# Performance work log

Measured on AMD Instinct MI355X. Metric: run time of the kernel, lower is better.

## Reference

```python
import jax, jax.numpy as jnp
import numpy as np

GROUPS = 32
EPS = 1e-5   # nn.GroupNorm default


def group_norm(x, gamma, beta):
    # x: [B, C, H, W]
    b, c, h, w = x.shape
    xg = x.reshape(b, GROUPS, c // GROUPS, h, w)
    mu = jnp.mean(xg, axis=(2, 3, 4), keepdims=True)
    var = jnp.var(xg, axis=(2, 3, 4), keepdims=True)
    xn = ((xg - mu) * jax.lax.rsqrt(var + EPS)).reshape(b, c, h, w)
    return xn * gamma[None, :, None, None] + beta[None, :, None, None]


def conv1x1(x, w, b):
    # x: [B, C, H, W], w: [O, C], b: [O]
    return jnp.einsum('bchw,oc->bohw', x, w) + b[None, :, None, None]


def setup_inputs() -> dict:
    key = jax.random.key(0)
    ks = jax.random.split(key, 10)
    B, C, H, W = 8, 512, 64, 64
    std = 1.0 / np.sqrt(C)
    inp = {
        'x': jax.random.normal(ks[0], (B, C, H, W), dtype=jnp.float32),
        'gn_gamma': jnp.ones((C,), dtype=jnp.float32),
        'gn_beta': jnp.zeros((C,), dtype=jnp.float32),
        'wq': jax.random.normal(ks[1], (C, C), dtype=jnp.float32) * std,
        'bq': jnp.zeros((C,), dtype=jnp.float32),
        'wk': jax.random.normal(ks[2], (C, C), dtype=jnp.float32) * std,
        'bk': jnp.zeros((C,), dtype=jnp.float32),
        'wv': jax.random.normal(ks[3], (C, C), dtype=jnp.float32) * std,
        'bv': jnp.zeros((C,), dtype=jnp.float32),
        'wp': jax.random.normal(ks[4], (C, C), dtype=jnp.float32) * std,
        'bp': jnp.zeros((C,), dtype=jnp.float32),
    }
    return inp


def reference(x, gn_gamma, gn_beta, wq, bq, wk, bk, wv, bv, wp, bp):
    b, c, hh, ww = x.shape
    n = hh * ww
    h = group_norm(x, gn_gamma, gn_beta)
    q = conv1x1(h, wq, bq).reshape(b, c, n).transpose(0, 2, 1)  # [B, N, C]
    k = conv1x1(h, wk, bk).reshape(b, c, n)                     # [B, C, N]
    v = conv1x1(h, wv, bv).reshape(b, c, n).transpose(0, 2, 1)  # [B, N, C]
    scale = 1.0 / jnp.sqrt(jnp.asarray(c, dtype=x.dtype))
    attn = jax.nn.softmax(jnp.einsum('bnc,bcm->bnm', q, k) * scale, axis=-1)
    out = jnp.einsum('bnm,bmc->bnc', attn, v)                   # [B, N, C]
    out = out.transpose(0, 2, 1).reshape(b, c, hh, ww)
    return x + conv1x1(out, wp, bp)
```

## Files before the change

### kernel.cpp

```cpp
#include <hip/hip_runtime.h>


typedef __attribute__((ext_vector_type(8))) __bf16 bf16x8;
typedef __attribute__((ext_vector_type(4))) float f32x4;
typedef unsigned int u32;

#define DEVICE __device__ __forceinline__

DEVICE void async_copy16(const void* g, void* l) {
  __builtin_amdgcn_global_load_lds(
      (__attribute__((address_space(1))) u32*)(g),
      (__attribute__((address_space(3))) u32*)(l),
      16, 0, 0);
}

__global__ __launch_bounds__(256) void cvt_w(
    const float* __restrict__ w0, const float* __restrict__ w1,
    const float* __restrict__ w2, const float* __restrict__ w3,
    __bf16* __restrict__ o0, __bf16* __restrict__ o1,
    __bf16* __restrict__ o2, __bf16* __restrict__ o3) {
  int idx = blockIdx.x * 256 + threadIdx.x;
  int off = idx * 8;
  int m = off >> 18;
  int r = off & 262143;
  const float* src = m == 0 ? w0 : m == 1 ? w1 : m == 2 ? w2 : w3;
  __bf16* dst = m == 0 ? o0 : m == 1 ? o1 : m == 2 ? o2 : o3;
  float4 a = *(const float4*)(src + r);
  float4 b = *(const float4*)(src + r + 4);
  bf16x8 v = {(__bf16)a.x, (__bf16)a.y, (__bf16)a.z, (__bf16)a.w,
              (__bf16)b.x, (__bf16)b.y, (__bf16)b.z, (__bf16)b.w};
  *(bf16x8*)(dst + r) = v;
}

__global__ __launch_bounds__(256) void gn_stats(const float* __restrict__ x,
                                                float* __restrict__ stats) {
  int bg = blockIdx.x;
  const float* p = x + (size_t)bg * 65536;
  int t = threadIdx.x, lane = t & 63, w = t >> 6;
  float s = 0.f, ss = 0.f;
  for (int i = t; i < 16384; i += 256) {
    float4 v = *(const float4*)(p + i * 4);
    s += v.x + v.y + v.z + v.w;
    ss += v.x * v.x + v.y * v.y + v.z * v.z + v.w * v.w;
  }
#pragma unroll
  for (int off = 32; off; off >>= 1) {
    s += __shfl_xor(s, off);
    ss += __shfl_xor(ss, off);
  }
  __shared__ float rs_[4], rss_[4];
  if (lane == 0) { rs_[w] = s; rss_[w] = ss; }
  __syncthreads();
  if (t == 0) {
    float S = rs_[0] + rs_[1] + rs_[2] + rs_[3];
    float SS = rss_[0] + rss_[1] + rss_[2] + rss_[3];
    float mean = S * (1.0f / 65536.0f);
    float var = SS * (1.0f / 65536.0f) - mean * mean;
    stats[bg * 2] = mean;
    stats[bg * 2 + 1] = rsqrtf(var + 1e-5f);
  }
}

__global__ __launch_bounds__(256) void gn_apply(
    const float* __restrict__ x, const float* __restrict__ gamma,
    const float* __restrict__ beta, const float* __restrict__ stats,
    __bf16* __restrict__ h) {
  int b = blockIdx.z, g = blockIdx.y;
  int n = blockIdx.x * 256 + threadIdx.x;
  const float* px = x + ((size_t)b * 512 + g * 16) * 4096 + n;
  float mean = stats[(b * 32 + g) * 2];
  float rstd = stats[(b * 32 + g) * 2 + 1];
  bf16x8 lo, hi;
#pragma unroll
  for (int c = 0; c < 8; ++c) {
    float v = px[(size_t)c * 4096];
    lo[c] = (__bf16)((v - mean) * rstd * gamma[g * 16 + c] + beta[g * 16 + c]);
  }
#pragma unroll
  for (int c = 0; c < 8; ++c) {
    float v = px[(size_t)(c + 8) * 4096];
    hi[c] = (__bf16)((v - mean) * rstd * gamma[g * 16 + c + 8] + beta[g * 16 + c + 8]);
  }
  __bf16* dst = h + ((size_t)b * 4096 + n) * 512 + g * 16;
  *(bf16x8*)dst = lo;
  *(bf16x8*)(dst + 8) = hi;
}


#define G256_PHASE(BUF, QR, QC, RDA, RDB, STAGE_STMT, TAIL_STMT)               \
  do {                                                                         \
    if (RDA) {                                                                 \
      _Pragma("unroll") for (int fr = 0; fr < 4; ++fr) {                       \
        a[fr][0] = ldA(BUF, (QR)*4 + fr, 0);                                   \
        a[fr][1] = ldA(BUF, (QR)*4 + fr, 1);                                   \
      }                                                                        \
    }                                                                          \
    if (RDB) {                                                                 \
      _Pragma("unroll") for (int fc = 0; fc < 2; ++fc) {                       \
        b[(QC)*2 + fc][0] = ldB(BUF, (QC)*2 + fc, 0);                          \
        b[(QC)*2 + fc][1] = ldB(BUF, (QC)*2 + fc, 1);                          \
      }                                                                        \
    }                                                                          \
    STAGE_STMT;                                                                \
    __builtin_amdgcn_s_barrier();                                              \
    asm volatile("s_waitcnt lgkmcnt(0)" ::: "memory");                         \
    __builtin_amdgcn_sched_barrier(0);                                         \
    __builtin_amdgcn_s_setprio(1);                                             \
    _Pragma("unroll") for (int fr = 0; fr < 4; ++fr)                           \
      _Pragma("unroll") for (int fc = 0; fc < 2; ++fc) {                       \
        acc[(QR)*4 + fr][(QC)*2 + fc] =                                        \
            __builtin_amdgcn_mfma_f32_16x16x32_bf16(                           \
                a[fr][0], b[(QC)*2 + fc][0], acc[(QR)*4 + fr][(QC)*2 + fc],    \
                0, 0, 0);                                                      \
        acc[(QR)*4 + fr][(QC)*2 + fc] =                                        \
            __builtin_amdgcn_mfma_f32_16x16x32_bf16(                           \
                a[fr][1], b[(QC)*2 + fc][1], acc[(QR)*4 + fr][(QC)*2 + fc],    \
                0, 0, 0);                                                      \
      }                                                                        \
    __builtin_amdgcn_s_setprio(0);                                             \
    TAIL_STMT;                                                                 \
    __builtin_amdgcn_sched_barrier(0);                                         \
    __builtin_amdgcn_s_barrier();                                              \
  } while (0)

#define G256_ITER(T0, T1, LAST)                                                \
  G256_PHASE(0, 0, 0, 1, 1, stage(1, 0, 0, (T1)), ((void)0));                  \
  G256_PHASE(0, 0, 1, 0, 1, stage(1, 0, 1, (T1)), ((void)0));                  \
  G256_PHASE(0, 1, 0, 1, 0,                                                    \
             if (!(LAST)) stage(0, 1, 0, (T0) + 2), ((void)0));                \
  G256_PHASE(0, 1, 1, 0, 0,                                                    \
             if (!(LAST)) stage(0, 1, 1, (T0) + 2),                            \
             if (LAST) {                                                       \
               asm volatile("s_waitcnt vmcnt(0)" ::: "memory");                \
             } else {                                                          \
               asm volatile("s_waitcnt vmcnt(4)" ::: "memory");                \
             });                                                               \
  G256_PHASE(1, 0, 0, 1, 1,                                                    \
             if (!(LAST)) stage(0, 0, 0, (T0) + 2), ((void)0));                \
  G256_PHASE(1, 0, 1, 0, 1,                                                    \
             if (!(LAST)) stage(0, 0, 1, (T0) + 2), ((void)0));                \
  G256_PHASE(1, 1, 0, 1, 0,                                                    \
             if (!(LAST)) stage(1, 1, 0, (T1) + 2), ((void)0));                \
  G256_PHASE(1, 1, 1, 0, 0,                                                    \
             if (!(LAST)) stage(1, 1, 1, (T1) + 2),                            \
             if (!(LAST)) {                                                    \
               asm volatile("s_waitcnt vmcnt(4)" ::: "memory");                \
             })

template <int EPI>
__global__ __launch_bounds__(512, 2) void gemm256(
    const __bf16* __restrict__ A, const __bf16* __restrict__ B,
    void* __restrict__ CoutV, int lda, int ldb, int ldc, int nIter, int nTM,
    int nTN, int KS, long sA, long sKA, long sB, long sKB, long sC,
    const float* __restrict__ bias0, const float* __restrict__ bias1,
    const float* __restrict__ resid) {
  __shared__ __bf16 lds_raw[2][2][2][128][64];

  int nwg = gridDim.x, bid = blockIdx.x;
  int qq = nwg >> 3, rr = nwg & 7;
  int xcd = bid & 7, ii = bid >> 3;
  int swz = (xcd < rr ? xcd * (qq + 1) : rr * (qq + 1) + (xcd - rr) * qq) + ii;
  int tn = swz % nTN;
  int tm = (swz / nTN) % nTM;
  int zz = swz / (nTN * nTM);
  int z = zz / KS, ks = zz % KS;
  A += (size_t)z * sA + (size_t)ks * sKA;
  B += (size_t)z * sB + (size_t)ks * sKB;
  __bf16* Cout = (__bf16*)CoutV + (size_t)zz * sC;
  int row0 = tm * 256, col0 = tn * 256;

  int tid = threadIdx.x;
  int wid = tid >> 6, lane = tid & 63;
  int wr = wid >> 2, wc = wid & 3;
  int l15 = lane & 15, l4 = lane >> 4;

  auto stage = [&](int buf, int mat, int half, int kt) {
    const __bf16* src = mat ? B : A;
    int ld = mat ? ldb : lda;
    int rbase = (mat ? col0 : row0) + half * 128;
    char* ldsbase = (char*)lds_raw + (((buf * 2 + mat) * 2 + half) * 16384);
#pragma unroll
    for (int L = 0; L < 2; ++L) {
      int ci = L * 512 + tid;
      int r = ci >> 3, cslot = ci & 7;
      int csrc = cslot ^ (r & 7);
      async_copy16(src + (size_t)(rbase + r) * ld + kt * 64 + csrc * 8,
                   ldsbase + (L * 512 + wid * 64) * 16);
    }
  };
  auto ldA = [&](int buf, int fr, int kh) -> bf16x8 {
    int row = fr * 16 + l15;
    int g = kh * 4 + l4;
    char* base = (char*)lds_raw + (((buf * 2 + 0) * 2 + wr) * 16384);
    return *(const bf16x8*)(base + row * 128 + ((g ^ (row & 7)) * 16));
  };
  auto ldB = [&](int buf, int fc, int kh) -> bf16x8 {
    int row = (wc & 1) * 64 + fc * 16 + l15;
    int g = kh * 4 + l4;
    char* base = (char*)lds_raw + (((buf * 2 + 1) * 2 + (wc >> 1)) * 16384);
    return *(const bf16x8*)(base + row * 128 + ((g ^ (row & 7)) * 16));
  };

  f32x4 acc[8][4] = {};
  bf16x8 a[4][2], b[4][2];

  stage(0, 1, 0, 0);
  stage(0, 1, 1, 0);
  stage(0, 0, 0, 0);
  stage(0, 0, 1, 0);
  stage(1, 1, 0, 1);
  stage(1, 1, 1, 1);
  asm volatile("s_waitcnt vmcnt(4)" ::: "memory");
  __builtin_amdgcn_sched_barrier(0);
  __builtin_amdgcn_s_barrier();

  int it = 0;
  for (; it < nIter - 1; ++it) {
    G256_ITER(2 * it, 2 * it + 1, 0);
  }
  G256_ITER(2 * it, 2 * it + 1, 1);

  int rb = row0 + wr * 128, cb = col0 + wc * 64;
#pragma unroll
  for (int fr = 0; fr < 8; ++fr) {
#pragma unroll
    for (int fc = 0; fc < 4; ++fc) {
      int col = cb + fc * 16 + l15;
      if constexpr (EPI == 3) {
        int r0 = rb + fr * 16 + l4 * 4;
        size_t idx = ((size_t)(r0 >> 12) * 512 + col) * 4096 + (r0 & 4095);
        float4 rv = *(const float4*)(resid + idx);
        float bb = bias0[col];
        float4 ov = {acc[fr][fc][0] + bb + rv.x, acc[fr][fc][1] + bb + rv.y,
                     acc[fr][fc][2] + bb + rv.z, acc[fr][fc][3] + bb + rv.w};
        *(float4*)((float*)CoutV + idx) = ov;
      } else {
        float cbias = 0.f;
        if constexpr (EPI == 1)
          cbias = col < 512 ? bias0[col] : bias1[col - 512];
#pragma unroll
        for (int rg = 0; rg < 4; ++rg) {
          int row = rb + fr * 16 + l4 * 4 + rg;
          float v = acc[fr][fc][rg];
          if constexpr (EPI == 1) v += cbias;
          if constexpr (EPI == 2) v += bias0[row];
          Cout[(size_t)row * ldc + col] = (__bf16)v;
        }
      }
    }
  }
}

__global__ __launch_bounds__(256) void softmax_rows_bf16(__bf16* __restrict__ S) {
  int row = blockIdx.x;
  __bf16* p = S + (size_t)row * 4096;
  int t = threadIdx.x, lane = t & 63, w = t >> 6;
  const float c1 = 0.04419417382415922f * 1.4426950408889634f;
  bf16x8 v0 = *(const bf16x8*)(p + t * 16);
  bf16x8 v1 = *(const bf16x8*)(p + t * 16 + 8);
  float f[16];
  float mx = -3.4e38f;
#pragma unroll
  for (int i = 0; i < 8; ++i) { f[i] = (float)v0[i]; mx = fmaxf(mx, f[i]); }
#pragma unroll
  for (int i = 0; i < 8; ++i) { f[8 + i] = (float)v1[i]; mx = fmaxf(mx, f[8 + i]); }
#pragma unroll
  for (int off = 32; off; off >>= 1) mx = fmaxf(mx, __shfl_xor(mx, off));
  __shared__ float rm[4], rsum[4];
  if (lane == 0) rm[w] = mx;
  __syncthreads();
  float m = fmaxf(fmaxf(rm[0], rm[1]), fmaxf(rm[2], rm[3]));
  float s = 0.f;
#pragma unroll
  for (int i = 0; i < 16; ++i) {
    f[i] = exp2f((f[i] - m) * c1);
    s += f[i];
  }
#pragma unroll
  for (int off = 32; off; off >>= 1) s += __shfl_xor(s, off);
  if (lane == 0) rsum[w] = s;
  __syncthreads();
  float inv = 1.0f / (rsum[0] + rsum[1] + rsum[2] + rsum[3]);
  bf16x8 o0, o1;
#pragma unroll
  for (int i = 0; i < 8; ++i) o0[i] = (__bf16)(f[i] * inv);
#pragma unroll
  for (int i = 0; i < 8; ++i) o1[i] = (__bf16)(f[8 + i] * inv);
  *(bf16x8*)(p + t * 16) = o0;
  *(bf16x8*)(p + t * 16 + 8) = o1;
}

__global__ __launch_bounds__(256) void reduce4(const __bf16* __restrict__ part,
                                               __bf16* __restrict__ out) {
  int z = blockIdx.y;
  size_t e = ((size_t)blockIdx.x * 256 + threadIdx.x) * 8;
  const __bf16* p = part + (size_t)z * 4 * 2097152 + e;
  bf16x8 v0 = *(const bf16x8*)(p);
  bf16x8 v1 = *(const bf16x8*)(p + 2097152);
  bf16x8 v2 = *(const bf16x8*)(p + 2 * 2097152);
  bf16x8 v3 = *(const bf16x8*)(p + 3 * 2097152);
  bf16x8 o;
#pragma unroll
  for (int j = 0; j < 8; ++j)
    o[j] = (__bf16)((float)v0[j] + (float)v1[j] + (float)v2[j] + (float)v3[j]);
  *(bf16x8*)(out + (size_t)z * 2097152 + e) = o;
}

extern "C" void kernel_launch(void* const* d_in, const int* in_sizes, int n_in,
                              void* d_out, int out_size, void* d_ws, size_t ws_size,
                              hipStream_t stream) {
  const float* x = (const float*)d_in[0];
  const float* gamma = (const float*)d_in[1];
  const float* beta = (const float*)d_in[2];
  const float* wq = (const float*)d_in[3];
  const float* bq = (const float*)d_in[4];
  const float* wk = (const float*)d_in[5];
  const float* bk = (const float*)d_in[6];
  const float* wv = (const float*)d_in[7];
  const float* bv = (const float*)d_in[8];
  const float* wp = (const float*)d_in[9];
  const float* bp = (const float*)d_in[10];

  char* p = (char*)d_ws;
  auto alloc = [&](size_t bytes) {
    char* r = p;
    p += (bytes + 255) & ~(size_t)255;
    return r;
  };
  float* stats = (float*)alloc(256 * 2 * 4);
  __bf16* wqkb = (__bf16*)alloc((size_t)1024 * 512 * 2);
  __bf16* wvb = (__bf16*)alloc(512 * 512 * 2);
  __bf16* wpb = (__bf16*)alloc(512 * 512 * 2);
  __bf16* ho = (__bf16*)alloc((size_t)8 * 4096 * 512 * 2);
  __bf16* qk = (__bf16*)alloc((size_t)8 * 4096 * 1024 * 2);
  __bf16* vt = (__bf16*)alloc((size_t)8 * 512 * 4096 * 2);

  const size_t SB = (size_t)4096 * 4096 * 2;
  const size_t PB = (size_t)4 * 4096 * 512 * 2;
  size_t used = (size_t)(p - (char*)d_ws);
  size_t freeb = (ws_size > used) ? ws_size - used : 0;
  int nb = (int)(freeb / (SB + PB));
  if (nb > 8) nb = 8;
  if (nb < 1) nb = 1;
  __bf16* s = (__bf16*)alloc(SB * nb);
  __bf16* pvp = (__bf16*)alloc(PB * nb);

  cvt_w<<<512, 256, 0, stream>>>(wq, wk, wv, wp, wqkb, wqkb + 262144, wvb, wpb);
  gn_stats<<<256, 256, 0, stream>>>(x, stats);
  gn_apply<<<dim3(16, 32, 8), 256, 0, stream>>>(x, gamma, beta, stats, ho);

  gemm256<1><<<dim3(512), 512, 0, stream>>>(
      ho, wqkb, qk, 512, 512, 1024, 4, 128, 4, 1, 0, 0, 0, 0, 0, bq, bk, nullptr);
  gemm256<2><<<dim3(256), 512, 0, stream>>>(
      wvb, ho, vt, 512, 512, 4096, 4, 2, 16, 1, 0, 0, 2097152, 0, 2097152,
      bv, nullptr, nullptr);

  __bf16* o = ho;
  for (int b0 = 0; b0 < 8; b0 += nb) {
    int zb = (8 - b0 < nb) ? (8 - b0) : nb;
    gemm256<0><<<dim3(zb * 256), 512, 0, stream>>>(
        qk + (size_t)b0 * 4194304, qk + (size_t)b0 * 4194304 + 512, s, 1024,
        1024, 4096, 4, 16, 16, 1, 4194304, 0, 4194304, 0, 16777216,
        nullptr, nullptr, nullptr);
    softmax_rows_bf16<<<zb * 4096, 256, 0, stream>>>(s);
    gemm256<0><<<dim3(zb * 128), 512, 0, stream>>>(
        s, vt + (size_t)b0 * 2097152, pvp, 4096, 4096, 512, 8, 16, 2, 4,
        16777216, 1024, 2097152, 1024, 2097152, nullptr, nullptr, nullptr);
    reduce4<<<dim3(1024, zb), 256, 0, stream>>>(pvp, o + (size_t)b0 * 2097152);
  }
  gemm256<3><<<dim3(256), 512, 0, stream>>>(
      o, wpb, d_out, 512, 512, 0, 4, 128, 2, 1, 0, 0, 0, 0, 0, bp, nullptr, x);
}
```

Measured before the change: 609.7 us.

## Split GEMM tile across sixteen waves with 64x64 per-wave subtiles

The 256x256-tile GEMM kernel now launches 1024 threads (16 waves in a 4x4 grid) instead of 512. Each wave computes a 64x64 output subtile instead of 128x64, and each thread issues one async global-to-LDS copy per stage instead of two. The vmcnt waits are lowered to match, and the launch bounds become (1024, 4). The aim is more waves to hide latency and fewer accumulator registers per wave. In exchange, each wave reuses its LDS fragments less, so there are more LDS reads per MFMA, and the strict launch-bounds hint may squeeze registers enough to cause spills.

Measured after the change: 914.8 us. 1.5x slower.

```diff
diff --git a/kernel.cpp b/kernel.cpp
--- a/kernel.cpp
+++ b/kernel.cpp
@@ -90,15 +90,15 @@
 #define G256_PHASE(BUF, QR, QC, RDA, RDB, STAGE_STMT, TAIL_STMT)               \
   do {                                                                         \
     if (RDA) {                                                                 \
-      _Pragma("unroll") for (int fr = 0; fr < 4; ++fr) {                       \
-        a[fr][0] = ldA(BUF, (QR)*4 + fr, 0);                                   \
-        a[fr][1] = ldA(BUF, (QR)*4 + fr, 1);                                   \
+      _Pragma("unroll") for (int fp = 0; fp < 2; ++fp) {                       \
+        a[fp][0] = ldA(BUF, (QR)*2 + fp, 0);                                   \
+        a[fp][1] = ldA(BUF, (QR)*2 + fp, 1);                                   \
       }                                                                        \
     }                                                                          \
     if (RDB) {                                                                 \
-      _Pragma("unroll") for (int fc = 0; fc < 2; ++fc) {                       \
-        b[(QC)*2 + fc][0] = ldB(BUF, (QC)*2 + fc, 0);                          \
-        b[(QC)*2 + fc][1] = ldB(BUF, (QC)*2 + fc, 1);                          \
+      _Pragma("unroll") for (int fp = 0; fp < 2; ++fp) {                       \
+        b[(QC)*2 + fp][0] = ldB(BUF, (QC)*2 + fp, 0);                          \
+        b[(QC)*2 + fp][1] = ldB(BUF, (QC)*2 + fp, 1);                          \
       }                                                                        \
     }                                                                          \
     STAGE_STMT;                                                                \
@@ -106,15 +106,15 @@
     asm volatile("s_waitcnt lgkmcnt(0)" ::: "memory");                         \
     __builtin_amdgcn_sched_barrier(0);                                         \
     __builtin_amdgcn_s_setprio(1);                                             \
-    _Pragma("unroll") for (int fr = 0; fr < 4; ++fr)                           \
-      _Pragma("unroll") for (int fc = 0; fc < 2; ++fc) {                       \
-        acc[(QR)*4 + fr][(QC)*2 + fc] =                                        \
+    _Pragma("unroll") for (int fp = 0; fp < 2; ++fp)                           \
+      _Pragma("unroll") for (int fq = 0; fq < 2; ++fq) {                       \
+        acc[(QR)*2 + fp][(QC)*2 + fq] =                                        \
             __builtin_amdgcn_mfma_f32_16x16x32_bf16(                           \
-                a[fr][0], b[(QC)*2 + fc][0], acc[(QR)*4 + fr][(QC)*2 + fc],    \
+                a[fp][0], b[(QC)*2 + fq][0], acc[(QR)*2 + fp][(QC)*2 + fq],    \
                 0, 0, 0);                                                      \
-        acc[(QR)*4 + fr][(QC)*2 + fc] =                                        \
+        acc[(QR)*2 + fp][(QC)*2 + fq] =                                        \
             __builtin_amdgcn_mfma_f32_16x16x32_bf16(                           \
-                a[fr][1], b[(QC)*2 + fc][1], acc[(QR)*4 + fr][(QC)*2 + fc],    \
+                a[fp][1], b[(QC)*2 + fq][1], acc[(QR)*2 + fp][(QC)*2 + fq],    \
                 0, 0, 0);                                                      \
       }                                                                        \
     __builtin_amdgcn_s_setprio(0);                                             \
@@ -133,7 +133,7 @@
              if (LAST) {                                                       \
                asm volatile("s_waitcnt vmcnt(0)" ::: "memory");                \
              } else {                                                          \
-               asm volatile("s_waitcnt vmcnt(4)" ::: "memory");                \
+               asm volatile("s_waitcnt vmcnt(2)" ::: "memory");                \
              });                                                               \
   G256_PHASE(1, 0, 0, 1, 1,                                                    \
              if (!(LAST)) stage(0, 0, 0, (T0) + 2), ((void)0));                \
@@ -144,11 +144,11 @@
   G256_PHASE(1, 1, 1, 0, 0,                                                    \
              if (!(LAST)) stage(1, 1, 1, (T1) + 2),                            \
              if (!(LAST)) {                                                    \
-               asm volatile("s_waitcnt vmcnt(4)" ::: "memory");                \
+               asm volatile("s_waitcnt vmcnt(2)" ::: "memory");                \
              })
 
 template <int EPI>
-__global__ __launch_bounds__(512, 2) void gemm256(
+__global__ __launch_bounds__(1024, 4) void gemm256(
     const __bf16* __restrict__ A, const __bf16* __restrict__ B,
     void* __restrict__ CoutV, int lda, int ldb, int ldc, int nIter, int nTM,
     int nTN, int KS, long sA, long sKA, long sB, long sKB, long sC,
@@ -179,19 +179,15 @@
     int ld = mat ? ldb : lda;
     int rbase = (mat ? col0 : row0) + half * 128;
     char* ldsbase = (char*)lds_raw + (((buf * 2 + mat) * 2 + half) * 16384);
-#pragma unroll
-    for (int L = 0; L < 2; ++L) {
-      int ci = L * 512 + tid;
-      int r = ci >> 3, cslot = ci & 7;
-      int csrc = cslot ^ (r & 7);
-      async_copy16(src + (size_t)(rbase + r) * ld + kt * 64 + csrc * 8,
-                   ldsbase + (L * 512 + wid * 64) * 16);
-    }
+    int r = tid >> 3, cslot = tid & 7;
+    int csrc = cslot ^ (r & 7);
+    async_copy16(src + (size_t)(rbase + r) * ld + kt * 64 + csrc * 8,
+                 ldsbase + tid * 16);
   };
   auto ldA = [&](int buf, int fr, int kh) -> bf16x8 {
-    int row = fr * 16 + l15;
+    int row = (wr & 1) * 64 + fr * 16 + l15;
     int g = kh * 4 + l4;
-    char* base = (char*)lds_raw + (((buf * 2 + 0) * 2 + wr) * 16384);
+    char* base = (char*)lds_raw + (((buf * 2 + 0) * 2 + (wr >> 1)) * 16384);
     return *(const bf16x8*)(base + row * 128 + ((g ^ (row & 7)) * 16));
   };
   auto ldB = [&](int buf, int fc, int kh) -> bf16x8 {
@@ -201,8 +197,8 @@
     return *(const bf16x8*)(base + row * 128 + ((g ^ (row & 7)) * 16));
   };
 
-  f32x4 acc[8][4] = {};
-  bf16x8 a[4][2], b[4][2];
+  f32x4 acc[4][4] = {};
+  bf16x8 a[2][2], b[4][2];
 
   stage(0, 1, 0, 0);
   stage(0, 1, 1, 0);
@@ -210,7 +206,7 @@
   stage(0, 0, 1, 0);
   stage(1, 1, 0, 1);
   stage(1, 1, 1, 1);
-  asm volatile("s_waitcnt vmcnt(4)" ::: "memory");
+  asm volatile("s_waitcnt vmcnt(2)" ::: "memory");
   __builtin_amdgcn_sched_barrier(0);
   __builtin_amdgcn_s_barrier();
 
@@ -220,9 +216,9 @@
   }
   G256_ITER(2 * it, 2 * it + 1, 1);
 
-  int rb = row0 + wr * 128, cb = col0 + wc * 64;
-#pragma unroll
-  for (int fr = 0; fr < 8; ++fr) {
+  int rb = row0 + wr * 64, cb = col0 + wc * 64;
+#pragma unroll
+  for (int fr = 0; fr < 4; ++fr) {
 #pragma unroll
     for (int fc = 0; fc < 4; ++fc) {
       int col = cb + fc * 16 + l15;
@@ -349,25 +345,25 @@
   gn_stats<<<256, 256, 0, stream>>>(x, stats);
   gn_apply<<<dim3(16, 32, 8), 256, 0, stream>>>(x, gamma, beta, stats, ho);
 
-  gemm256<1><<<dim3(512), 512, 0, stream>>>(
+  gemm256<1><<<dim3(512), 1024, 0, stream>>>(
       ho, wqkb, qk, 512, 512, 1024, 4, 128, 4, 1, 0, 0, 0, 0, 0, bq, bk, nullptr);
-  gemm256<2><<<dim3(256), 512, 0, stream>>>(
+  gemm256<2><<<dim3(256), 1024, 0, stream>>>(
       wvb, ho, vt, 512, 512, 4096, 4, 2, 16, 1, 0, 0, 2097152, 0, 2097152,
       bv, nullptr, nullptr);
 
   __bf16* o = ho;
   for (int b0 = 0; b0 < 8; b0 += nb) {
     int zb = (8 - b0 < nb) ? (8 - b0) : nb;
-    gemm256<0><<<dim3(zb * 256), 512, 0, stream>>>(
+    gemm256<0><<<dim3(zb * 256), 1024, 0, stream>>>(
         qk + (size_t)b0 * 4194304, qk + (size_t)b0 * 4194304 + 512, s, 1024,
         1024, 4096, 4, 16, 16, 1, 4194304, 0, 4194304, 0, 16777216,
         nullptr, nullptr, nullptr);
     softmax_rows_bf16<<<zb * 4096, 256, 0, stream>>>(s);
-    gemm256<0><<<dim3(zb * 128), 512, 0, stream>>>(
+    gemm256<0><<<dim3(zb * 128), 1024, 0, stream>>>(
         s, vt + (size_t)b0 * 2097152, pvp, 4096, 4096, 512, 8, 16, 2, 4,
         16777216, 1024, 2097152, 1024, 2097152, nullptr, nullptr, nullptr);
     reduce4<<<dim3(1024, zb), 256, 0, stream>>>(pvp, o + (size_t)b0 * 2097152);
   }
-  gemm256<3><<<dim3(256), 512, 0, stream>>>(
+  gemm256<3><<<dim3(256), 1024, 0, stream>>>(
       o, wpb, d_out, 512, 512, 0, 4, 128, 2, 1, 0, 0, 0, 0, 0, bp, nullptr, x);
 }
```
